# Optimization experiments

Measured on AMD Instinct MI355X. Metric: run time of the kernel, lower is better.

## Reference

```python
import jax, jax.numpy as jnp
import numpy as np

G = 32           # number of graphs
NODES = 256      # nodes per graph (equal-sized graphs)
P = 8            # primary capsules per node
IN_DIM = 128     # primary capsule dim
O = 16           # out_caps
OUT_DIM = 128    # out capsule dim
SDIM = OUT_DIM // 2
V = 16           # vector channels
R = 3            # routing iterations


def squash(t, axis=-1):
    sn = jnp.sum(t * t, axis=axis, keepdims=True)
    scale = sn / (1.0 + sn)
    return scale * t / (jnp.sqrt(sn) + 1e-8)


def setup_inputs() -> dict:
    key = jax.random.key(0)
    ks = jax.random.split(key, 4)
    N = G * NODES
    x = jax.random.normal(ks[0], (N, P, IN_DIM), dtype=jnp.float32)
    x_vectors = jax.random.normal(ks[1], (N, V, 3), dtype=jnp.float32)
    W_scalar = jax.random.normal(ks[2], (O, IN_DIM // 2, SDIM), dtype=jnp.float32)
    W_vector = jax.random.normal(ks[3], (O, IN_DIM // 2, OUT_DIM - SDIM), dtype=jnp.float32)
    bias = jnp.zeros((O, OUT_DIM), dtype=jnp.float32)
    batch = jnp.repeat(jnp.arange(G, dtype=jnp.int64), NODES)  # contiguous equal-size graphs
    return {"x": x, "x_vectors": x_vectors, "W_scalar": W_scalar,
            "W_vector": W_vector, "bias": bias, "batch": batch}


def reference(x, x_vectors, W_scalar, W_vector, bias, batch):
    # Equal-size contiguous graphs -> per-graph masking == reshape to [G, NODES, ...]
    xg = x.reshape(G, NODES, P, IN_DIM)
    xvg = x_vectors.reshape(G, NODES, V, 3)

    def per_graph(xb, xvb):
        scalar_part = xb[..., : IN_DIM // 2]           # [n, P, D/2]
        vector_part = xb[..., IN_DIM // 2:]
        u_s = jnp.einsum('npd,ods->npos', scalar_part, W_scalar)
        u_v = jnp.einsum('npd,odv->npov', vector_part, W_vector)
        u = jnp.concatenate([u_s, u_v], axis=-1).reshape(NODES * P, O, OUT_DIM)

        b = jnp.zeros((NODES * P, O), dtype=xb.dtype)
        c = None
        v = None
        for it in range(R):
            c = jax.nn.softmax(b, axis=1)                     # [M, O]
            s_j = jnp.einsum('mo,mod->od', c, u) + bias       # [O, OUT_DIM]
            v = squash(s_j, axis=1)
            if it < R - 1:
                agreement = jnp.einsum('mos,os->mo', u[..., :SDIM], v[:, :SDIM])
                b = b + agreement

        cr = c.reshape(NODES, P, O)
        routed = jnp.einsum('npo,nvc->ovc', cr, xvb)          # [O, V, 3]
        return v, routed

    caps, vecs = jax.vmap(per_graph)(xg, xvg)
    return caps, vecs
```

## Files before the change

### kernel.cpp

```cpp
#include <hip/hip_runtime.h>

#define G_    32
#define O_    16
#define OUTD  128
#define DS_   64
#define VC    48
#define M_    2048
#define ROWS  128
#define CPG   16
#define XP    136
#define XPD   68
#define WVP   72
#define YLP   132

typedef __attribute__((ext_vector_type(8))) short short8;
typedef __attribute__((ext_vector_type(4))) float f32x4;

__device__ __forceinline__ unsigned short f2bf(float f) {
  unsigned u = __float_as_uint(f);
  return (unsigned short)((u + 0x7FFFu + ((u >> 16) & 1u)) >> 16);
}
__device__ __forceinline__ float bf2f(short v) {
  return __uint_as_float(((unsigned)(unsigned short)v) << 16);
}

__global__ __launch_bounds__(256) void stage_x(
    const float* __restrict__ x, short* __restrict__ xTg,
    float* __restrict__ ysum_part)
{
  const int blk = blockIdx.x;
  const int t = threadIdx.x;
  __shared__ short xT[128 * XP];

  const float* xg = x + (size_t)blk * (ROWS * OUTD);
  {
    const int rg = t >> 2, qc = t & 3;
    const float4* r0q = (const float4*)(xg + (size_t)(2 * rg) * OUTD + qc * 32);
    const float4* r1q = (const float4*)(xg + (size_t)(2 * rg + 1) * OUTD + qc * 32);
    float4 a0 = r0q[0], a1 = r0q[1], a2 = r0q[2], a3 = r0q[3],
           a4 = r0q[4], a5 = r0q[5], a6 = r0q[6], a7 = r0q[7];
    float4 b0 = r1q[0], b1 = r1q[1], b2 = r1q[2], b3 = r1q[3],
           b4 = r1q[4], b5 = r1q[5], b6 = r1q[6], b7 = r1q[7];
    unsigned* xTd = (unsigned*)xT;
    const int cb = qc * 32;
#define STAGE4(S, A, B)                                                        \
    xTd[(cb + S*4 + 0) * XPD + rg] = (unsigned)f2bf(A.x) | ((unsigned)f2bf(B.x) << 16); \
    xTd[(cb + S*4 + 1) * XPD + rg] = (unsigned)f2bf(A.y) | ((unsigned)f2bf(B.y) << 16); \
    xTd[(cb + S*4 + 2) * XPD + rg] = (unsigned)f2bf(A.z) | ((unsigned)f2bf(B.z) << 16); \
    xTd[(cb + S*4 + 3) * XPD + rg] = (unsigned)f2bf(A.w) | ((unsigned)f2bf(B.w) << 16);
    STAGE4(0, a0, b0) STAGE4(1, a1, b1) STAGE4(2, a2, b2) STAGE4(3, a3, b3)
    STAGE4(4, a4, b4) STAGE4(5, a5, b5) STAGE4(6, a6, b6) STAGE4(7, a7, b7)
#undef STAGE4
  }
  __syncthreads();

  {
    short8* dst = (short8*)(xTg + (size_t)blk * (128 * 128));
#pragma unroll
    for (int i = 0; i < 8; ++i) {
      int c = i * 256 + t;
      dst[c] = *(const short8*)&xT[(c >> 4) * XP + (c & 15) * 8];
    }
  }
  {
    const int k = t >> 1, half = t & 1;
    float s = 0.f;
#pragma unroll
    for (int j = 0; j < 8; ++j) {
      short8 v = *(const short8*)&xT[k * XP + half * 64 + j * 8];
#pragma unroll
      for (int e = 0; e < 8; ++e) s += bf2f(v[e]);
    }
    s += __shfl_xor(s, 1);
    if (half == 0) ysum_part[(size_t)blk * 128 + k] = s;
  }
}

template<int LAST>
__global__ __launch_bounds__(256) void capsA_t(
    const short* __restrict__ xTg, const float* __restrict__ xv,
    const float* __restrict__ wvacc, float* __restrict__ y_part,
    float* __restrict__ routed_part)
{
  const int blk = blockIdx.x, g = blk >> 4, chunk = blk & 15;
  const int t = threadIdx.x, lane = t & 63, w = t >> 6;

  __shared__ short xT[128 * XP];
  __shared__ short cT[O_ * XP];
  __shared__ short wv_s[O_ * WVP];
  __shared__ float cp_s[16][17];
  __shared__ float xv_s[16 * VC];
  __shared__ float y_lds[16 * YLP];

  {
    const short8* src = (const short8*)(xTg + (size_t)blk * (128 * 128));
#pragma unroll
    for (int i = 0; i < 8; ++i) {
      int c = i * 256 + t;
      *(short8*)&xT[(c >> 4) * XP + (c & 15) * 8] = src[c];
    }
  }
  {
    const float* wvg = wvacc + (size_t)g * O_ * DS_;
    for (int i = t; i < O_ * DS_; i += 256) {
      int o = i >> 6, k = i & 63;
      wv_s[o * WVP + k] = (short)f2bf(wvg[i]);
    }
  }
  if (LAST) {
    const float* xvg = xv + (size_t)(g * 256 + chunk * 16) * VC;
    for (int i = t; i < 16 * VC; i += 256) xv_s[i] = xvg[i];
  }
  __syncthreads();

  {
    const int mrow = lane & 15, gq = lane >> 4;
    float c_fA[4], c_fB[4];
#define LOGIT_TILE(NT2, CF)                                                    \
    {                                                                          \
      const int nt = 2 * w + NT2;                                              \
      const int mcol = nt * 16 + mrow;                                         \
      f32x4 acc = {0.f, 0.f, 0.f, 0.f};                                        \
      _Pragma("unroll")                                                        \
      for (int ks = 0; ks < 2; ++ks) {                                         \
        short8 af = *(const short8*)&wv_s[mrow * WVP + ks * 32 + gq * 8];      \
        short8 bf;                                                             \
        _Pragma("unroll")                                                      \
        for (int e = 0; e < 8; ++e)                                            \
          bf[e] = xT[(ks * 32 + gq * 8 + e) * XP + mcol];                      \
        acc = __builtin_amdgcn_mfma_f32_16x16x32_bf16(af, bf, acc, 0, 0, 0);   \
      }                                                                        \
      float mx = fmaxf(fmaxf(acc[0], acc[1]), fmaxf(acc[2], acc[3]));          \
      mx = fmaxf(mx, __shfl_xor(mx, 16));                                      \
      mx = fmaxf(mx, __shfl_xor(mx, 32));                                      \
      float e0 = __expf(acc[0] - mx), e1 = __expf(acc[1] - mx);                \
      float e2 = __expf(acc[2] - mx), e3 = __expf(acc[3] - mx);                \
      float sm = e0 + e1 + e2 + e3;                                            \
      sm += __shfl_xor(sm, 16);                                                \
      sm += __shfl_xor(sm, 32);                                                \
      float inv = 1.f / sm;                                                    \
      CF[0] = e0 * inv; CF[1] = e1 * inv; CF[2] = e2 * inv; CF[3] = e3 * inv;  \
      cT[(gq * 4 + 0) * XP + mcol] = (short)f2bf(CF[0]);                       \
      cT[(gq * 4 + 1) * XP + mcol] = (short)f2bf(CF[1]);                       \
      cT[(gq * 4 + 2) * XP + mcol] = (short)f2bf(CF[2]);                       \
      cT[(gq * 4 + 3) * XP + mcol] = (short)f2bf(CF[3]);                       \
    }
    LOGIT_TILE(0, c_fA)
    LOGIT_TILE(1, c_fB)
#undef LOGIT_TILE

    if (LAST) {
#define CP_TILE(NT2, CF)                                                       \
      {                                                                        \
        const int nt = 2 * w + NT2;                                            \
        _Pragma("unroll")                                                      \
        for (int r = 0; r < 4; ++r) {                                          \
          float v = CF[r];                                                     \
          v += __shfl_xor(v, 1); v += __shfl_xor(v, 2); v += __shfl_xor(v, 4); \
          if ((lane & 7) == 0)                                                 \
            cp_s[nt * 2 + ((lane >> 3) & 1)][gq * 4 + r] = v;                  \
        }                                                                      \
      }
      CP_TILE(0, c_fA)
      CP_TILE(1, c_fB)
#undef CP_TILE
    }
  }
  __syncthreads();

  {
    const int oc = lane & 15, gq = lane >> 4;
    f32x4 y0 = {0.f, 0.f, 0.f, 0.f}, y1 = {0.f, 0.f, 0.f, 0.f};
#pragma unroll
    for (int ks = 0; ks < 4; ++ks) {
      short8 bf = *(const short8*)&cT[oc * XP + ks * 32 + gq * 8];
      short8 a0 = *(const short8*)&xT[((2 * w + 0) * 16 + oc) * XP + ks * 32 + gq * 8];
      short8 a1 = *(const short8*)&xT[((2 * w + 1) * 16 + oc) * XP + ks * 32 + gq * 8];
      y0 = __builtin_amdgcn_mfma_f32_16x16x32_bf16(a0, bf, y0, 0, 0, 0);
      y1 = __builtin_amdgcn_mfma_f32_16x16x32_bf16(a1, bf, y1, 0, 0, 0);
    }
#pragma unroll
    for (int r = 0; r < 4; ++r) {
      y_lds[oc * YLP + (2 * w + 0) * 16 + gq * 4 + r] = y0[r];
      y_lds[oc * YLP + (2 * w + 1) * 16 + gq * 4 + r] = y1[r];
    }
  }
  __syncthreads();
  {
    float* yp = y_part + (size_t)(g * CPG + chunk) * 2048;
    const int oo = t >> 4, k8 = (t & 15) * 8;
    float4 q0 = *(const float4*)&y_lds[oo * YLP + k8];
    float4 q1 = *(const float4*)&y_lds[oo * YLP + k8 + 4];
    *(float4*)&yp[t * 8] = q0;
    *(float4*)&yp[t * 8 + 4] = q1;
  }

  if (LAST) {
    float* rp = routed_part + (size_t)(g * CPG + chunk) * 768;
#pragma unroll
    for (int e = 0; e < 3; ++e) {
      int idx = t + 256 * e;
      int o = idx / VC, j = idx % VC;
      float acc = 0.f;
#pragma unroll
      for (int n = 0; n < 16; ++n) acc += cp_s[n][o] * xv_s[n * VC + j];
      rp[idx] = acc;
    }
  }
}

template<int FIRST, int LAST>
__global__ __launch_bounds__(256) void capsB_t(
    const float* __restrict__ y_part, const float* __restrict__ ysum_part,
    const float* __restrict__ Ws, const float* __restrict__ Wv,
    const float* __restrict__ bias, float* __restrict__ wvacc,
    float* __restrict__ caps, const float* __restrict__ routed_part,
    float* __restrict__ vecs)
{
  const int b = blockIdx.x, g = b >> 3, osub = b & 7, t = threadIdx.x;
  __shared__ float y_s[2][128];
  __shared__ float v_s[2][64];
  __shared__ float pn_s[4];

  if (FIRST) {
    if (t < 128) {
      float s = 0.f;
#pragma unroll
      for (int ch = 0; ch < CPG; ++ch)
        s += ysum_part[(size_t)(g * CPG + ch) * 128 + t];
      s *= 0.0625f;
      y_s[0][t] = s;
      y_s[1][t] = s;
    }
  } else {
    const int o2 = t >> 7, k = t & 127;
    const float* yp = y_part + (size_t)g * CPG * 2048 + (osub * 2 + o2) * 128 + k;
    float s = 0.f;
#pragma unroll
    for (int ch = 0; ch < CPG; ++ch) s += yp[ch * 2048];
    y_s[o2][k] = s;
  }
  __syncthreads();

  const int ol = t >> 7, d = t & 127, o = osub * 2 + ol;
  const float* W = (d < 64) ? (Ws + (size_t)o * 64 * 64 + d)
                            : (Wv + (size_t)o * 64 * 64 + (d - 64));
  const int kbase = (d < 64) ? 0 : 64;
  float s = 0.f;
#pragma unroll
  for (int k = 0; k < 64; ++k) s += y_s[ol][kbase + k] * W[k * 64];
  s += bias[o * OUTD + d];

  float pn = s * s;
#pragma unroll
  for (int m = 1; m < 64; m <<= 1) pn += __shfl_xor(pn, m);
  if ((t & 63) == 0) pn_s[t >> 6] = pn;
  __syncthreads();
  float sn = pn_s[ol * 2] + pn_s[ol * 2 + 1];
  float f = sn / ((1.f + sn) * (sqrtf(sn) + 1e-8f));
  float v = f * s;
  if (d < 64) v_s[ol][d] = v;
  if (LAST) caps[((size_t)g * O_ + o) * OUTD + d] = v;
  __syncthreads();

  if (!LAST) {
    if (t < 128) {
      int ol2 = t >> 6, k = t & 63, o2 = osub * 2 + ol2;
      const float* Wr = Ws + ((size_t)o2 * 64 + k) * 64;
      float acc = 0.f;
#pragma unroll
      for (int ss = 0; ss < 64; ss += 4) {
        float4 wq = *(const float4*)(Wr + ss);
        float4 vq = *(const float4*)&v_s[ol2][ss];
        acc += wq.x * vq.x + wq.y * vq.y + wq.z * vq.z + wq.w * vq.w;
      }
      float* wa = wvacc + ((size_t)g * O_ + o2) * 64 + k;
      *wa = (FIRST ? 0.f : *wa) + acc;
    }
  } else {
    if (t < 96) {
      int idx = osub * 96 + t;
      const float* rp = routed_part + (size_t)g * CPG * 768 + idx;
      float s2 = 0.f;
#pragma unroll
      for (int ch = 0; ch < CPG; ++ch) s2 += rp[ch * 768];
      vecs[(size_t)g * 768 + idx] = s2;
    }
  }
}

extern "C" void kernel_launch(void* const* d_in, const int* in_sizes, int n_in,
                              void* d_out, int out_size, void* d_ws, size_t ws_size,
                              hipStream_t stream)
{
  const float* x    = (const float*)d_in[0];
  const float* xv   = (const float*)d_in[1];
  const float* Ws   = (const float*)d_in[2];
  const float* Wv   = (const float*)d_in[3];
  const float* bias = (const float*)d_in[4];

  float* out  = (float*)d_out;
  float* caps = out;
  float* vecs = out + (size_t)G_ * O_ * OUTD;

  float* ws          = (float*)d_ws;
  float* wvacc       = ws;
  float* y_part      = ws + (size_t)G_ * O_ * DS_;
  float* routed_part = y_part + (size_t)G_ * CPG * 128 * 16;
  float* ysum_part   = routed_part + (size_t)G_ * CPG * 768;
  short* xTg         = (short*)(ysum_part + (size_t)G_ * CPG * 128);

  dim3 blk(256), grdA(G_ * CPG), grdB(G_ * 8);

  stage_x<<<grdA, blk, 0, stream>>>(x, xTg, ysum_part);
  capsB_t<1, 0><<<grdB, blk, 0, stream>>>(y_part, ysum_part, Ws, Wv, bias,
                                          wvacc, caps, routed_part, vecs);
  capsA_t<0><<<grdA, blk, 0, stream>>>(xTg, xv, wvacc, y_part, routed_part);
  capsB_t<0, 0><<<grdB, blk, 0, stream>>>(y_part, ysum_part, Ws, Wv, bias,
                                          wvacc, caps, routed_part, vecs);
  capsA_t<1><<<grdA, blk, 0, stream>>>(xTg, xv, wvacc, y_part, routed_part);
  capsB_t<0, 1><<<grdB, blk, 0, stream>>>(y_part, ysum_part, Ws, Wv, bias,
                                          wvacc, caps, routed_part, vecs);
}
```

Baseline: 43.88 us.

## Replace per-chunk partial buffers with atomic accumulation and widen capsB grid

The partial sums from stage_x and capsA are now accumulated with float atomics into per-graph buffers, which a single memset zeroes up front. This removes the 16-way partial-sum reduction loops in capsB. capsB now launches one block per (graph, out-capsule) instead of per pair, and splits the K reduction across two thread halves, giving more blocks and shorter serial loops. In exchange it adds an extra memset launch, atomic contention (16 chunks per address), and nondeterministic summation order.

```diff
diff --git a/kernel.cpp b/kernel.cpp
--- a/kernel.cpp
+++ b/kernel.cpp
@@ -26,9 +26,9 @@
 
 __global__ __launch_bounds__(256) void stage_x(
     const float* __restrict__ x, short* __restrict__ xTg,
-    float* __restrict__ ysum_part)
+    float* __restrict__ ysum)
 {
-  const int blk = blockIdx.x;
+  const int blk = blockIdx.x, g = blk >> 4;
   const int t = threadIdx.x;
   __shared__ short xT[128 * XP];
 
@@ -72,15 +72,15 @@
       for (int e = 0; e < 8; ++e) s += bf2f(v[e]);
     }
     s += __shfl_xor(s, 1);
-    if (half == 0) ysum_part[(size_t)blk * 128 + k] = s;
+    if (half == 0) unsafeAtomicAdd(&ysum[(size_t)g * 128 + k], s);
   }
 }
 
 template<int LAST>
 __global__ __launch_bounds__(256) void capsA_t(
     const short* __restrict__ xTg, const float* __restrict__ xv,
-    const float* __restrict__ wvacc, float* __restrict__ y_part,
-    float* __restrict__ routed_part)
+    const float* __restrict__ wvacc, float* __restrict__ y_out,
+    float* __restrict__ routed)
 {
   const int blk = blockIdx.x, g = blk >> 4, chunk = blk & 15;
   const int t = threadIdx.x, lane = t & 63, w = t >> 6;
@@ -187,16 +187,16 @@
   }
   __syncthreads();
   {
-    float* yp = y_part + (size_t)(g * CPG + chunk) * 2048;
+    float* yp = y_out + (size_t)g * (O_ * OUTD);
     const int oo = t >> 4, k8 = (t & 15) * 8;
-    float4 q0 = *(const float4*)&y_lds[oo * YLP + k8];
-    float4 q1 = *(const float4*)&y_lds[oo * YLP + k8 + 4];
-    *(float4*)&yp[t * 8] = q0;
-    *(float4*)&yp[t * 8 + 4] = q1;
+    const float* sp = &y_lds[oo * YLP + k8];
+#pragma unroll
+    for (int e = 0; e < 8; ++e)
+      unsafeAtomicAdd(&yp[oo * OUTD + k8 + e], sp[e]);
   }
 
   if (LAST) {
-    float* rp = routed_part + (size_t)(g * CPG + chunk) * 768;
+    float* rp = routed + (size_t)g * 768;
 #pragma unroll
     for (int e = 0; e < 3; ++e) {
       int idx = t + 256 * e;
@@ -204,87 +204,85 @@
       float acc = 0.f;
 #pragma unroll
       for (int n = 0; n < 16; ++n) acc += cp_s[n][o] * xv_s[n * VC + j];
-      rp[idx] = acc;
+      unsafeAtomicAdd(&rp[idx], acc);
     }
   }
 }
 
 template<int FIRST, int LAST>
 __global__ __launch_bounds__(256) void capsB_t(
-    const float* __restrict__ y_part, const float* __restrict__ ysum_part,
+    const float* __restrict__ y_in, const float* __restrict__ ysum,
     const float* __restrict__ Ws, const float* __restrict__ Wv,
     const float* __restrict__ bias, float* __restrict__ wvacc,
-    float* __restrict__ caps, const float* __restrict__ routed_part,
+    float* __restrict__ caps, const float* __restrict__ routed,
     float* __restrict__ vecs)
 {
-  const int b = blockIdx.x, g = b >> 3, osub = b & 7, t = threadIdx.x;
-  __shared__ float y_s[2][128];
-  __shared__ float v_s[2][64];
-  __shared__ float pn_s[4];
-
-  if (FIRST) {
-    if (t < 128) {
-      float s = 0.f;
-#pragma unroll
-      for (int ch = 0; ch < CPG; ++ch)
-        s += ysum_part[(size_t)(g * CPG + ch) * 128 + t];
-      s *= 0.0625f;
-      y_s[0][t] = s;
-      y_s[1][t] = s;
-    }
-  } else {
-    const int o2 = t >> 7, k = t & 127;
-    const float* yp = y_part + (size_t)g * CPG * 2048 + (osub * 2 + o2) * 128 + k;
-    float s = 0.f;
-#pragma unroll
-    for (int ch = 0; ch < CPG; ++ch) s += yp[ch * 2048];
-    y_s[o2][k] = s;
-  }
-  __syncthreads();
-
-  const int ol = t >> 7, d = t & 127, o = osub * 2 + ol;
-  const float* W = (d < 64) ? (Ws + (size_t)o * 64 * 64 + d)
-                            : (Wv + (size_t)o * 64 * 64 + (d - 64));
-  const int kbase = (d < 64) ? 0 : 64;
-  float s = 0.f;
-#pragma unroll
-  for (int k = 0; k < 64; ++k) s += y_s[ol][kbase + k] * W[k * 64];
-  s += bias[o * OUTD + d];
-
-  float pn = s * s;
-#pragma unroll
-  for (int m = 1; m < 64; m <<= 1) pn += __shfl_xor(pn, m);
-  if ((t & 63) == 0) pn_s[t >> 6] = pn;
-  __syncthreads();
-  float sn = pn_s[ol * 2] + pn_s[ol * 2 + 1];
-  float f = sn / ((1.f + sn) * (sqrtf(sn) + 1e-8f));
-  float v = f * s;
-  if (d < 64) v_s[ol][d] = v;
-  if (LAST) caps[((size_t)g * O_ + o) * OUTD + d] = v;
+  const int b = blockIdx.x, g = b >> 4, o = b & 15, t = threadIdx.x;
+  __shared__ float yB[128];
+  __shared__ float ps[2][128];
+  __shared__ float vB[64];
+  __shared__ float pn_s[2];
+
+  if (t < 128) {
+    yB[t] = FIRST ? ysum[(size_t)g * 128 + t] * 0.0625f
+                  : y_in[((size_t)g * O_ + o) * OUTD + t];
+  }
+  __syncthreads();
+
+  {
+    const int kh = t >> 7, d = t & 127;
+    const float* W = (d < 64) ? (Ws + (size_t)o * 4096 + d)
+                              : (Wv + (size_t)o * 4096 + (d - 64));
+    const int ybase = (d < 64) ? 0 : 64;
+    float a0 = 0.f, a1 = 0.f;
+#pragma unroll
+    for (int k = 0; k < 32; k += 2) {
+      const int kl = kh * 32 + k;
+      a0 += yB[ybase + kl] * W[(size_t)kl * 64];
+      a1 += yB[ybase + kl + 1] * W[(size_t)(kl + 1) * 64];
+    }
+    ps[kh][d] = a0 + a1;
+  }
+  __syncthreads();
+
+  float sv = 0.f;
+  if (t < 128) {
+    sv = ps[0][t] + ps[1][t] + bias[o * OUTD + t];
+    float pn = sv * sv;
+#pragma unroll
+    for (int m = 1; m < 64; m <<= 1) pn += __shfl_xor(pn, m);
+    if ((t & 63) == 0) pn_s[t >> 6] = pn;
+  }
+  __syncthreads();
+  if (t < 128) {
+    float sn = pn_s[0] + pn_s[1];
+    float f = sn / ((1.f + sn) * (sqrtf(sn) + 1e-8f));
+    float v = f * sv;
+    if (t < 64) vB[t] = v;
+    if (LAST) caps[((size_t)g * O_ + o) * OUTD + t] = v;
+  }
   __syncthreads();
 
   if (!LAST) {
     if (t < 128) {
-      int ol2 = t >> 6, k = t & 63, o2 = osub * 2 + ol2;
-      const float* Wr = Ws + ((size_t)o2 * 64 + k) * 64;
+      const int k = t >> 1, half = t & 1;
+      const float* Wr = Ws + ((size_t)o * 64 + k) * 64 + half * 32;
       float acc = 0.f;
 #pragma unroll
-      for (int ss = 0; ss < 64; ss += 4) {
+      for (int ss = 0; ss < 32; ss += 4) {
         float4 wq = *(const float4*)(Wr + ss);
-        float4 vq = *(const float4*)&v_s[ol2][ss];
+        float4 vq = *(const float4*)&vB[half * 32 + ss];
         acc += wq.x * vq.x + wq.y * vq.y + wq.z * vq.z + wq.w * vq.w;
       }
-      float* wa = wvacc + ((size_t)g * O_ + o2) * 64 + k;
-      *wa = (FIRST ? 0.f : *wa) + acc;
+      acc += __shfl_xor(acc, 1);
+      if (half == 0) {
+        float* wa = wvacc + ((size_t)g * O_ + o) * 64 + k;
+        *wa = (FIRST ? 0.f : *wa) + acc;
+      }
     }
   } else {
-    if (t < 96) {
-      int idx = osub * 96 + t;
-      const float* rp = routed_part + (size_t)g * CPG * 768 + idx;
-      float s2 = 0.f;
-#pragma unroll
-      for (int ch = 0; ch < CPG; ++ch) s2 += rp[ch * 768];
-      vecs[(size_t)g * 768 + idx] = s2;
+    if (t < 48) {
+      vecs[(size_t)g * 768 + o * VC + t] = routed[(size_t)g * 768 + o * VC + t];
     }
   }
 }
@@ -303,22 +301,26 @@
   float* caps = out;
   float* vecs = out + (size_t)G_ * O_ * OUTD;
 
-  float* ws          = (float*)d_ws;
-  float* wvacc       = ws;
-  float* y_part      = ws + (size_t)G_ * O_ * DS_;
-  float* routed_part = y_part + (size_t)G_ * CPG * 128 * 16;
-  float* ysum_part   = routed_part + (size_t)G_ * CPG * 768;
-  short* xTg         = (short*)(ysum_part + (size_t)G_ * CPG * 128);
-
-  dim3 blk(256), grdA(G_ * CPG), grdB(G_ * 8);
-
-  stage_x<<<grdA, blk, 0, stream>>>(x, xTg, ysum_part);
-  capsB_t<1, 0><<<grdB, blk, 0, stream>>>(y_part, ysum_part, Ws, Wv, bias,
-                                          wvacc, caps, routed_part, vecs);
-  capsA_t<0><<<grdA, blk, 0, stream>>>(xTg, xv, wvacc, y_part, routed_part);
-  capsB_t<0, 0><<<grdB, blk, 0, stream>>>(y_part, ysum_part, Ws, Wv, bias,
-                                          wvacc, caps, routed_part, vecs);
-  capsA_t<1><<<grdA, blk, 0, stream>>>(xTg, xv, wvacc, y_part, routed_part);
-  capsB_t<0, 1><<<grdB, blk, 0, stream>>>(y_part, ysum_part, Ws, Wv, bias,
-                                          wvacc, caps, routed_part, vecs);
-}
+  float* ws     = (float*)d_ws;
+  float* wvacc  = ws;
+  float* ysum   = ws + 32768;
+  float* y1     = ysum + 4096;
+  float* y2     = y1 + 65536;
+  float* routed = y2 + 65536;
+  short* xTg    = (short*)(routed + 24576);
+
+  hipMemsetAsync((void*)ysum, 0, (4096 + 65536 + 65536 + 24576) * sizeof(float),
+                 stream);
+
+  dim3 blk(256), grdA(G_ * CPG), grdB(G_ * O_);
+
+  stage_x<<<grdA, blk, 0, stream>>>(x, xTg, ysum);
+  capsB_t<1, 0><<<grdB, blk, 0, stream>>>(y1, ysum, Ws, Wv, bias, wvacc,
+                                          caps, routed, vecs);
+  capsA_t<0><<<grdA, blk, 0, stream>>>(xTg, xv, wvacc, y1, routed);
+  capsB_t<0, 0><<<grdB, blk, 0, stream>>>(y1, ysum, Ws, Wv, bias, wvacc,
+                                          caps, routed, vecs);
+  capsA_t<1><<<grdA, blk, 0, stream>>>(xTg, xv, wvacc, y2, routed);
+  capsB_t<0, 1><<<grdB, blk, 0, stream>>>(y2, ysum, Ws, Wv, bias, wvacc,
+                                          caps, routed, vecs);
+}
```

After: 96.82 us. 2.21x slower.
